# Performance work log

Hardware: AMD Instinct MI355X
Metric: run time of the kernel (lower is better)

## Reference

```python
import jax, jax.numpy as jnp
import numpy as np

N, C, T = 64, 128, 2048
S = 9          # shift_size
D = 1          # dilation
EPS = 1e-5


def setup_inputs() -> dict:
    key = jax.random.key(0)
    k1, k2 = jax.random.split(key)
    x = jax.random.normal(k1, (N, C, T), dtype=jnp.float32)
    conv_w = jax.random.normal(k2, (C, S), dtype=jnp.float32) * (1.0 / np.sqrt(S))
    gamma = jnp.ones((C,), dtype=jnp.float32)
    beta = jnp.zeros((C,), dtype=jnp.float32)
    return {"x": x, "conv_w": conv_w, "gamma": gamma, "beta": beta}


def reference(x, conv_w, gamma, beta):
    n, c, t = x.shape
    s = conv_w.shape[1]
    # --- per-channel temporal shift with zero fill (vectorized shift()) ---
    sh = ((jnp.arange(c) % s) - s // 2) * D                    # [C]
    idx = jnp.arange(t)[None, :] - sh[:, None]                 # [C, T] source index
    valid = (idx >= 0) & (idx < t)
    idxc = jnp.clip(idx, 0, t - 1)
    xs = jnp.take_along_axis(x, jnp.broadcast_to(idxc[None], (n, c, t)), axis=2)
    xs = jnp.where(valid[None], xs, 0.0)                       # [N, C, T]
    # --- zero-pad channel dim then unfold windows of size S, stride 1 (q=1) ---
    pad_top = s // 2
    pad_bot = s // 2 - (1 if s % 2 == 0 else 0)
    xp = jnp.pad(xs, ((0, 0), (pad_top, pad_bot), (0, 0)))     # [N, C+pads, T]
    win_idx = jnp.arange(c)[:, None] + jnp.arange(s)[None, :]  # [C, S]
    w = xp[:, win_idx, :]                                      # [N, C, S, T]
    # --- grouped 1x1 conv: each output channel i mixes its S-window ---
    out = jnp.einsum('ncst,cs->nct', w, conv_w)                # [N, C, T]
    # --- BatchNorm1d (training-mode batch stats, biased var) + ReLU ---
    mean = out.mean(axis=(0, 2), keepdims=True)
    var = ((out - mean) ** 2).mean(axis=(0, 2), keepdims=True)
    out = (out - mean) * jax.lax.rsqrt(var + EPS)
    out = out * gamma[None, :, None] + beta[None, :, None]
    return jax.nn.relu(out)
```

## Files before the change

### kernel.cpp

```cpp
#include <hip/hip_runtime.h>

#define NN 64
#define CC 128
#define TT 2048
#define SS 9
#define PAD 4
#define EPSF 1e-5f
#define TL 32
#define NT 2
#define TPB (NT * TL)
#define ROWS (CC + 2 * PAD)
#define STRIDE 36
#define NB 16


union H8 { _Float16 h[8]; uint4 u; };

__device__ __forceinline__ void tile_load(
    const float* __restrict__ xn, const int tb, const int tid,
    const bool interior, float4 (&v)[5])
{
#pragma unroll
    for (int p = 0; p < 5; ++p) {
        const int f = tid + 256 * p;
        const int r = f >> 3;
        v[p] = make_float4(0.f, 0.f, 0.f, 0.f);
        if (r < ROWS) {
            const int c2 = r - PAD;
            if (c2 >= 0 && c2 < CC) {
                const int j0 = (f & 7) * 4;
                const int sh = c2 % SS - PAD;
                const int t  = tb + j0 - sh;
                const float* __restrict__ row = xn + (size_t)c2 * TT;
                if (interior) {
                    __builtin_memcpy(&v[p], row + t, sizeof(float4));
                } else {
                    v[p].x = (t     >= 0 && t     < TT) ? row[t]     : 0.f;
                    v[p].y = (t + 1 >= 0 && t + 1 < TT) ? row[t + 1] : 0.f;
                    v[p].z = (t + 2 >= 0 && t + 2 < TT) ? row[t + 2] : 0.f;
                    v[p].w = (t + 3 >= 0 && t + 3 < TT) ? row[t + 3] : 0.f;
                }
            }
        }
    }
}

__device__ __forceinline__ void tile_write(
    float* __restrict__ ls, const int tid, const float4 (&v)[5])
{
#pragma unroll
    for (int p = 0; p < 5; ++p) {
        const int f = tid + 256 * p;
        const int r = f >> 3;
        if (r < ROWS)
            *reinterpret_cast<float4*>(&ls[r * STRIDE + (f & 7) * 4]) = v[p];
    }
}

__device__ __forceinline__ void conv_tile(
    const float* __restrict__ ls, const int base, const float (&wv)[SS],
    float (&res)[16])
{
#pragma unroll
    for (int j = 0; j < 16; ++j) res[j] = 0.f;
#pragma unroll
    for (int s = 0; s < SS; ++s) {
        const float4* rp = reinterpret_cast<const float4*>(&ls[base + s * STRIDE]);
        float4 r0 = rp[0], r1 = rp[1], r2 = rp[2], r3 = rp[3];
        const float w = wv[s];
        res[0]  = fmaf(w, r0.x, res[0]);  res[1]  = fmaf(w, r0.y, res[1]);
        res[2]  = fmaf(w, r0.z, res[2]);  res[3]  = fmaf(w, r0.w, res[3]);
        res[4]  = fmaf(w, r1.x, res[4]);  res[5]  = fmaf(w, r1.y, res[5]);
        res[6]  = fmaf(w, r1.z, res[6]);  res[7]  = fmaf(w, r1.w, res[7]);
        res[8]  = fmaf(w, r2.x, res[8]);  res[9]  = fmaf(w, r2.y, res[9]);
        res[10] = fmaf(w, r2.z, res[10]); res[11] = fmaf(w, r2.w, res[11]);
        res[12] = fmaf(w, r3.x, res[12]); res[13] = fmaf(w, r3.y, res[13]);
        res[14] = fmaf(w, r3.z, res[14]); res[15] = fmaf(w, r3.w, res[15]);
    }
}

__device__ __forceinline__ void store_f16(
    unsigned short* __restrict__ hrow, const int off, const float (&res)[16])
{
    H8 p0, p1;
#pragma unroll
    for (int j = 0; j < 8; ++j) {
        p0.h[j] = (_Float16)res[j];
        p1.h[j] = (_Float16)res[8 + j];
    }
    *reinterpret_cast<uint4*>(hrow + off)     = p0.u;
    *reinterpret_cast<uint4*>(hrow + off + 8) = p1.u;
}

__global__ __launch_bounds__(256, 4) void conv_stats_f16(
    const float* __restrict__ x, const float* __restrict__ cw,
    float* __restrict__ buckets, float* __restrict__ out)
{
    __shared__ float ls[ROWS * STRIDE];

    const int n   = blockIdx.y;
    const int tA  = blockIdx.x * TPB;
    const int tB  = tA + TL;
    const int tid = threadIdx.x;
    const float* __restrict__ xn = x + (size_t)n * CC * TT;

    float4 va[5];
    tile_load(xn, tA, tid, blockIdx.x != 0, va);
    tile_write(ls, tid, va);

    const int c  = tid & (CC - 1);
    const int jb = (tid >> 7) * (TL / 2);
    float wv[SS];
#pragma unroll
    for (int s = 0; s < SS; ++s) wv[s] = cw[c * SS + s];
    unsigned short* __restrict__ hrow =
        reinterpret_cast<unsigned short*>(out + ((size_t)n * CC + c) * TT);

    __syncthreads();

    float4 vb[5];
    tile_load(xn, tB, tid, (int)blockIdx.x != (int)gridDim.x - 1, vb);

    const int base = c * STRIDE + jb;
    float res[16];
    conv_tile(ls, base, wv, res);
    float s1 = 0.f, s2 = 0.f;
#pragma unroll
    for (int j = 0; j < 16; ++j) { s1 += res[j]; s2 = fmaf(res[j], res[j], s2); }
    store_f16(hrow, tA + jb, res);

    __syncthreads();
    tile_write(ls, tid, vb);
    __syncthreads();

    conv_tile(ls, base, wv, res);
#pragma unroll
    for (int j = 0; j < 16; ++j) { s1 += res[j]; s2 = fmaf(res[j], res[j], s2); }
    store_f16(hrow, tB + jb, res);

    __syncthreads();
    ls[tid]       = s1;
    ls[256 + tid] = s2;
    __syncthreads();
    if (tid < CC) {
        float* bs = buckets + ((blockIdx.x + blockIdx.y) & (NB - 1)) * 2 * CC;
        atomicAdd(&bs[tid],      ls[tid]       + ls[tid + 128]);
        atomicAdd(&bs[CC + tid], ls[256 + tid] + ls[256 + tid + 128]);
    }
}

__global__ __launch_bounds__(256, 8) void norm_relu_f16(
    const float* __restrict__ buckets, const float* __restrict__ gamma,
    const float* __restrict__ beta, float* __restrict__ out)
{
    const int r0  = blockIdx.x * 4;
    const int tid = threadIdx.x;

    float g[4], b[4];
#pragma unroll
    for (int k = 0; k < 4; ++k) {
        const int c = (r0 + k) & (CC - 1);
        float t1 = 0.f, t2 = 0.f;
#pragma unroll
        for (int kk = 0; kk < NB; ++kk) {
            t1 += buckets[kk * 2 * CC + c];
            t2 += buckets[kk * 2 * CC + CC + c];
        }
        const float inv_cnt = 1.0f / (float)(NN * TT);
        const float mean = t1 * inv_cnt;
        const float var  = t2 * inv_cnt - mean * mean;
        const float inv  = rsqrtf(var + EPSF);
        g[k] = gamma[c] * inv;
        b[k] = beta[c] - mean * g[k];
    }

    H8 hv[4];
#pragma unroll
    for (int k = 0; k < 4; ++k) {
        const unsigned short* hrow =
            reinterpret_cast<const unsigned short*>(out + (size_t)(r0 + k) * TT);
        hv[k].u = *reinterpret_cast<const uint4*>(hrow + 8 * tid);
    }
    __syncthreads();

#pragma unroll
    for (int k = 0; k < 4; ++k) {
        float4 lo, hi;
        lo.x = fmaf((float)hv[k].h[0], g[k], b[k]);
        lo.y = fmaf((float)hv[k].h[1], g[k], b[k]);
        lo.z = fmaf((float)hv[k].h[2], g[k], b[k]);
        lo.w = fmaf((float)hv[k].h[3], g[k], b[k]);
        hi.x = fmaf((float)hv[k].h[4], g[k], b[k]);
        hi.y = fmaf((float)hv[k].h[5], g[k], b[k]);
        hi.z = fmaf((float)hv[k].h[6], g[k], b[k]);
        hi.w = fmaf((float)hv[k].h[7], g[k], b[k]);
        lo.x = lo.x > 0.f ? lo.x : 0.f;
        lo.y = lo.y > 0.f ? lo.y : 0.f;
        lo.z = lo.z > 0.f ? lo.z : 0.f;
        lo.w = lo.w > 0.f ? lo.w : 0.f;
        hi.x = hi.x > 0.f ? hi.x : 0.f;
        hi.y = hi.y > 0.f ? hi.y : 0.f;
        hi.z = hi.z > 0.f ? hi.z : 0.f;
        hi.w = hi.w > 0.f ? hi.w : 0.f;
        float* row = out + (size_t)(r0 + k) * TT;
        *reinterpret_cast<float4*>(row + 8 * tid)     = lo;
        *reinterpret_cast<float4*>(row + 8 * tid + 4) = hi;
    }
}

extern "C" void kernel_launch(void* const* d_in, const int* in_sizes, int n_in,
                              void* d_out, int out_size, void* d_ws, size_t ws_size,
                              hipStream_t stream)
{
    const float* x     = (const float*)d_in[0];
    const float* cw    = (const float*)d_in[1];
    const float* gamma = (const float*)d_in[2];
    const float* beta  = (const float*)d_in[3];
    float* out     = (float*)d_out;
    float* buckets = (float*)d_ws;

    hipMemsetAsync(buckets, 0, (size_t)NB * 2 * CC * sizeof(float), stream);

    dim3 grid1(TT / TPB, NN);
    conv_stats_f16<<<grid1, 256, 0, stream>>>(x, cw, buckets, out);
    norm_relu_f16<<<(NN * CC) / 4, 256, 0, stream>>>(buckets, gamma, beta, out);
}
```

Baseline: 154.2 us.

## Store fp16 conv intermediates in tile-contiguous workspace and normalize per tile

The conv/stats kernel now writes its fp16 intermediate into a separate workspace buffer laid out per 32-column time tile, with each 16-element chunk stored contiguously across channels, instead of packing it into the output rows. A new normalize kernel reads these tiles with the same grid as the conv kernel, computes per-channel scale and shift once per block in shared memory, and writes fp32 output. The intent is to get contiguous, coalesced stores in the conv pass and to avoid the in-place read-then-overwrite on the output. In exchange it needs extra workspace and falls back to the old row-wise path when the workspace is too small.

New measurement: 278.4 us. +80.6%, slower.

```diff
diff --git a/kernel.cpp b/kernel.cpp
--- a/kernel.cpp
+++ b/kernel.cpp
@@ -15,6 +15,7 @@
 
 
 union H8 { _Float16 h[8]; uint4 u; };
+union H4 { _Float16 h[4]; uint2 u; };
 
 __device__ __forceinline__ void tile_load(
     const float* __restrict__ xn, const int tb, const int tid,
@@ -79,8 +80,10 @@
     }
 }
 
-__device__ __forceinline__ void store_f16(
-    unsigned short* __restrict__ hrow, const int off, const float (&res)[16])
+__device__ __forceinline__ void store_conv_f16(
+    _Float16* __restrict__ hb, unsigned short* __restrict__ hrow,
+    const int fast, const int tile_g, const int t0,
+    const int c, const int jb, const float (&res)[16])
 {
     H8 p0, p1;
 #pragma unroll
@@ -88,13 +91,21 @@
         p0.h[j] = (_Float16)res[j];
         p1.h[j] = (_Float16)res[8 + j];
     }
-    *reinterpret_cast<uint4*>(hrow + off)     = p0.u;
-    *reinterpret_cast<uint4*>(hrow + off + 8) = p1.u;
+    if (fast) {
+        _Float16* dst = hb + (size_t)tile_g * (CC * TL)
+                      + ((jb >> 4) * CC + c) * 16;
+        *reinterpret_cast<uint4*>(dst)     = p0.u;
+        *reinterpret_cast<uint4*>(dst + 8) = p1.u;
+    } else {
+        *reinterpret_cast<uint4*>(hrow + t0 + jb)     = p0.u;
+        *reinterpret_cast<uint4*>(hrow + t0 + jb + 8) = p1.u;
+    }
 }
 
 __global__ __launch_bounds__(256, 4) void conv_stats_f16(
     const float* __restrict__ x, const float* __restrict__ cw,
-    float* __restrict__ buckets, float* __restrict__ out)
+    float* __restrict__ buckets, _Float16* __restrict__ hb,
+    float* __restrict__ out, const int fast)
 {
     __shared__ float ls[ROWS * STRIDE];
 
@@ -115,6 +126,7 @@
     for (int s = 0; s < SS; ++s) wv[s] = cw[c * SS + s];
     unsigned short* __restrict__ hrow =
         reinterpret_cast<unsigned short*>(out + ((size_t)n * CC + c) * TT);
+    const int gA = n * (TT / TL) + (tA >> 5);
 
     __syncthreads();
 
@@ -127,7 +139,7 @@
     float s1 = 0.f, s2 = 0.f;
 #pragma unroll
     for (int j = 0; j < 16; ++j) { s1 += res[j]; s2 = fmaf(res[j], res[j], s2); }
-    store_f16(hrow, tA + jb, res);
+    store_conv_f16(hb, hrow, fast, gA, tA, c, jb, res);
 
     __syncthreads();
     tile_write(ls, tid, vb);
@@ -136,7 +148,7 @@
     conv_tile(ls, base, wv, res);
 #pragma unroll
     for (int j = 0; j < 16; ++j) { s1 += res[j]; s2 = fmaf(res[j], res[j], s2); }
-    store_f16(hrow, tB + jb, res);
+    store_conv_f16(hb, hrow, fast, gA + 1, tB, c, jb, res);
 
     __syncthreads();
     ls[tid]       = s1;
@@ -149,7 +161,64 @@
     }
 }
 
-__global__ __launch_bounds__(256, 8) void norm_relu_f16(
+__global__ __launch_bounds__(256, 8) void norm_tile(
+    const _Float16* __restrict__ hb, const float* __restrict__ buckets,
+    const float* __restrict__ gamma, const float* __restrict__ beta,
+    float* __restrict__ out)
+{
+    __shared__ float gs[CC], bs[CC];
+
+    const int n   = blockIdx.y;
+    const int tA  = blockIdx.x * TPB;
+    const int tid = threadIdx.x;
+
+    if (tid < CC) {
+        float t1 = 0.f, t2 = 0.f;
+#pragma unroll
+        for (int k = 0; k < NB; ++k) {
+            t1 += buckets[k * 2 * CC + tid];
+            t2 += buckets[k * 2 * CC + CC + tid];
+        }
+        const float inv_cnt = 1.0f / (float)(NN * TT);
+        const float mean = t1 * inv_cnt;
+        const float var  = t2 * inv_cnt - mean * mean;
+        const float inv  = rsqrtf(var + EPSF);
+        const float g    = gamma[tid] * inv;
+        gs[tid] = g;
+        bs[tid] = beta[tid] - mean * g;
+    }
+    __syncthreads();
+
+#pragma unroll
+    for (int tile = 0; tile < NT; ++tile) {
+        const int t0 = tA + tile * TL;
+        const _Float16* __restrict__ tb =
+            hb + (size_t)(n * (TT / TL) + (t0 >> 5)) * (CC * TL);
+        float* __restrict__ on = out + (size_t)n * CC * TT + t0;
+#pragma unroll
+        for (int k = 0; k < 4; ++k) {
+            const int f = tid + 256 * k;
+            const int r = f >> 3;
+            const int q = (f & 7) * 4;
+            H4 h;
+            h.u = *reinterpret_cast<const uint2*>(
+                tb + ((q >> 4) * CC + r) * 16 + (q & 15));
+            const float g = gs[r], b = bs[r];
+            float4 v;
+            v.x = fmaf((float)h.h[0], g, b);
+            v.y = fmaf((float)h.h[1], g, b);
+            v.z = fmaf((float)h.h[2], g, b);
+            v.w = fmaf((float)h.h[3], g, b);
+            v.x = v.x > 0.f ? v.x : 0.f;
+            v.y = v.y > 0.f ? v.y : 0.f;
+            v.z = v.z > 0.f ? v.z : 0.f;
+            v.w = v.w > 0.f ? v.w : 0.f;
+            *reinterpret_cast<float4*>(on + (size_t)r * TT + q) = v;
+        }
+    }
+}
+
+__global__ __launch_bounds__(256, 8) void norm_relu_rows(
     const float* __restrict__ buckets, const float* __restrict__ gamma,
     const float* __restrict__ beta, float* __restrict__ out)
 {
@@ -219,9 +288,18 @@
     float* out     = (float*)d_out;
     float* buckets = (float*)d_ws;
 
-    hipMemsetAsync(buckets, 0, (size_t)NB * 2 * CC * sizeof(float), stream);
+    const size_t bucket_bytes = (size_t)NB * 2 * CC * sizeof(float);
+    const size_t hb_bytes     = (size_t)NN * CC * TT * sizeof(_Float16);
+    const int fast = (ws_size >= bucket_bytes + hb_bytes) ? 1 : 0;
+    _Float16* hb = (_Float16*)((char*)d_ws + bucket_bytes);
+
+    hipMemsetAsync(buckets, 0, bucket_bytes, stream);
 
     dim3 grid1(TT / TPB, NN);
-    conv_stats_f16<<<grid1, 256, 0, stream>>>(x, cw, buckets, out);
-    norm_relu_f16<<<(NN * CC) / 4, 256, 0, stream>>>(buckets, gamma, beta, out);
-}
+    conv_stats_f16<<<grid1, 256, 0, stream>>>(x, cw, buckets, hb, out, fast);
+    if (fast) {
+        norm_tile<<<grid1, 256, 0, stream>>>(hb, buckets, gamma, beta, out);
+    } else {
+        norm_relu_rows<<<(NN * CC) / 4, 256, 0, stream>>>(buckets, gamma, beta, out);
+    }
+}
```
